# Kernel optimization log

Hardware: AMD Instinct MI355X
Metric: run time of the kernel (lower is better)

## Reference

```python
import jax, jax.numpy as jnp
import numpy as np

B, T, P = 64, 20, 36
V, E, H, D = 32000, 300, 512, 512


def setup_inputs() -> dict:
    key = jax.random.key(0)
    ks = jax.random.split(key, 12)
    s = lambda k, shape, scale=0.05: (jax.random.normal(k, shape, jnp.float32) * scale)
    inp = {
        "h0": jax.random.normal(ks[0], (B, H), jnp.float32),
        "object_proposals": jax.random.normal(ks[1], (B, P, D), jnp.float32),
        "captions": jax.random.randint(ks[2], (B, T), 0, V),
        # lengths in [2, T]; force one row to max so max(decode_lengths) == T-1 (static)
        "caption_lengths": jax.random.randint(ks[3], (B, 1), 2, T + 1).at[0, 0].set(T),
        "emb_W": s(ks[4], (V, E), 0.1),
        "W_ih": s(ks[5], (4 * H, E + D)),
        "W_hh": s(ks[6], (4 * H, H)),
        "b_ih": jnp.zeros((4 * H,), jnp.float32),
        "b_hh": jnp.zeros((4 * H,), jnp.float32),
        "wh_W": s(ks[7], (H, E)), "wh_b": jnp.zeros((H,), jnp.float32),
        "wr_W": s(ks[8], (D, E)), "wr_b": jnp.zeros((D,), jnp.float32),
        "rh_W": s(ks[9], (H, D)), "rh_b": jnp.zeros((H,), jnp.float32),
        "w_W": s(ks[10], (E,)), "w_b": jnp.zeros((), jnp.float32),
        "r_W": s(ks[11], (D,)), "r_b": jnp.zeros((), jnp.float32),
    }
    return inp


def reference(h0, object_proposals, captions, caption_lengths, emb_W,
              W_ih, W_hh, b_ih, b_hh, wh_W, wh_b, wr_W, wr_b,
              rh_W, rh_b, w_W, w_b, r_W, r_b):
    lengths = caption_lengths[:, 0]
    sort_ind = jnp.argsort(-lengths)  # descending, stable
    h0s = h0[sort_ind]
    props = object_proposals[sort_ind]           # [B,P,D]
    caps = captions[sort_ind]                    # [B,T]
    dec = lengths[sort_ind] - 1                  # decode lengths
    Tmax = captions.shape[1] - 1                 # == max(decode_lengths) by construction

    emb = emb_W[caps]                            # [B,T,E]
    # Loop-invariant projections of the full embedding matrix (done once, not per step)
    WH = emb_W @ wh_W.T + wh_b                   # [V,H]
    WRp = emb_W @ wr_W.T + wr_b                  # [V,D]
    w_lin = emb_W @ w_W + w_b                    # [V]
    sum_WH = WH.sum(0)                           # [H]
    sum_WRp = WRp.sum(0)                         # [D]
    sum_wlin = w_lin.sum()                       # scalar
    RH = props @ rh_W.T + rh_b                   # [B,P,H]
    r_lin = props @ r_W + r_b                    # [B,P]
    S = props.sum(1)                             # [B,D]  (sum over proposals)
    wr_sumP = S @ WRp.T                          # [B,V]  = sum_p wr[b,v,p]
    wr_sumV = props @ sum_WRp                    # [B,P]  = sum_v wr[b,v,p]

    xs = (jnp.swapaxes(emb[:, :Tmax], 0, 1), jnp.arange(Tmax))

    def step(carry, x):
        h, c, fb = carry
        e_t, t = x
        mask = (t < dec)[:, None].astype(h.dtype)  # [B,1] active rows
        xin = jnp.concatenate([e_t, fb], axis=1)   # [B,E+D]
        gates = xin @ W_ih.T + b_ih + h @ W_hh.T + b_hh
        i, f, g, o = jnp.split(gates, 4, axis=1)
        c_new = jax.nn.sigmoid(f) * c + jax.nn.sigmoid(i) * jnp.tanh(g)
        h_new = jax.nn.sigmoid(o) * jnp.tanh(c_new)
        w = h_new @ WH.T + w_lin                               # [B,V]
        r = jnp.einsum('bph,bh->bp', RH, h_new) + r_lin        # [B,P]
        preds = w + wr_sumP + r.sum(1, keepdims=True)          # [B,V]
        att_logits = (h_new @ sum_WH + sum_wlin)[:, None] + wr_sumV + r
        att = jax.nn.softmax(att_logits, axis=1)               # [B,P]
        fb_new = jnp.einsum('bp,bpd->bd', att, props)          # [B,D]
        h = mask * h_new + (1.0 - mask) * h
        c = mask * c_new + (1.0 - mask) * c
        fb = mask * fb_new + (1.0 - mask) * fb
        return (h, c, fb), (preds * mask, att * mask)

    init = (h0s, h0s, jnp.zeros((h0.shape[0], props.shape[2]), h0.dtype))
    _, (P_seq, A_seq) = jax.lax.scan(step, init, xs)
    predictions = jnp.swapaxes(P_seq, 0, 1)  # [B,Tmax,V]
    attention = jnp.swapaxes(A_seq, 0, 1)    # [B,Tmax,P]
    return predictions, attention, caps[:, 1:], dec, sort_ind
```

## Files before the change

### kernel.cpp

```cpp
#include <hip/hip_runtime.h>

typedef unsigned short u16;
typedef __bf16 bf16t;
typedef bf16t v8bf __attribute__((ext_vector_type(8)));
typedef float v4f __attribute__((ext_vector_type(4)));

#define Bb 64
#define Tt 20
#define Tm 19
#define Pp 36
#define Vv 32000
#define Ee 300
#define Ep 320
#define Hh 512
#define Dd 512
#define Gg 2048

__device__ __forceinline__ u16 f2b(float f) {
    unsigned u = __builtin_bit_cast(unsigned, f);
    unsigned r = u + 0x7fffu + ((u >> 16) & 1u);
    return (u16)(r >> 16);
}
__device__ __forceinline__ float b2f(u16 x) {
    return __builtin_bit_cast(float, (unsigned)x << 16);
}
__device__ __forceinline__ v8bf ld8(const u16* p) {
    return *reinterpret_cast<const v8bf*>(p);
}

__device__ __forceinline__ float ld_f32_coh(const float* p) {
    return __hip_atomic_load(p, __ATOMIC_RELAXED, __HIP_MEMORY_SCOPE_AGENT);
}
__device__ __forceinline__ void st_f32_coh(float* p, float v) {
    __hip_atomic_store(p, v, __ATOMIC_RELAXED, __HIP_MEMORY_SCOPE_AGENT);
}
__device__ __forceinline__ void st_u32_coh(unsigned* p, unsigned v) {
    __hip_atomic_store(p, v, __ATOMIC_RELAXED, __HIP_MEMORY_SCOPE_AGENT);
}

__global__ void k_sentinel_r4(float* __restrict__ out, float val)
{
    int i = blockIdx.x * 256 + threadIdx.x;
    if (i < 8192) out[i] = val;
}

template<int EPI>
__global__ __launch_bounds__(256) void gemm_bt_r4(
    const u16* __restrict__ A, const u16* __restrict__ B,
    int lda, int ldb, int K,
    float* __restrict__ Cf, u16* __restrict__ Cb, int ldc,
    const float* __restrict__ addN, const float* __restrict__ addM,
    const u16* __restrict__ addMatB,
    const u16* __restrict__ wspB, const int* __restrict__ dec,
    float* __restrict__ outP)
{
    int bn = blockIdx.x, bm = blockIdx.y;
    const int tid = threadIdx.x;
    const int w = tid >> 6, l = tid & 63;
    const int lr = l & 15, lk = (l >> 4) << 3;
    const int m0 = bm * 64;
    const int n0 = bn * 64 + w * 16;
    const u16* Ap = A + (size_t)(m0 + lr) * lda + lk;
    const u16* Bp = B + (size_t)(n0 + lr) * ldb + lk;
    v4f acc0 = {0.f,0.f,0.f,0.f}, acc1 = {0.f,0.f,0.f,0.f},
        acc2 = {0.f,0.f,0.f,0.f}, acc3 = {0.f,0.f,0.f,0.f};
    for (int k = 0; k < K; k += 32) {
        v8bf bf = ld8(Bp + k);
        v8bf a0 = ld8(Ap + k);
        v8bf a1 = ld8(Ap + (size_t)16 * lda + k);
        v8bf a2 = ld8(Ap + (size_t)32 * lda + k);
        v8bf a3 = ld8(Ap + (size_t)48 * lda + k);
        acc0 = __builtin_amdgcn_mfma_f32_16x16x32_bf16(a0, bf, acc0, 0, 0, 0);
        acc1 = __builtin_amdgcn_mfma_f32_16x16x32_bf16(a1, bf, acc1, 0, 0, 0);
        acc2 = __builtin_amdgcn_mfma_f32_16x16x32_bf16(a2, bf, acc2, 0, 0, 0);
        acc3 = __builtin_amdgcn_mfma_f32_16x16x32_bf16(a3, bf, acc3, 0, 0, 0);
    }
    v4f accs[4] = {acc0, acc1, acc2, acc3};
    const int crow0 = (l >> 4) * 4;
    const int n = n0 + lr;
    #pragma unroll
    for (int i = 0; i < 4; ++i) {
        #pragma unroll
        for (int r = 0; r < 4; ++r) {
            int m = m0 + i * 16 + crow0 + r;
            float v = accs[i][r];
            if (EPI == 0) {
                if (addN) v += addN[n];
                Cf[(size_t)m * ldc + n] = v;
            } else if (EPI == 1) {
                Cb[(size_t)m * ldc + n] = f2b(v);
            } else if (EPI == 4) {
                Cb[(size_t)m * ldc + n] = f2b(v + addN[n]);
            } else if (EPI == 5) {
                Cb[(size_t)m * ldc + n] = f2b(v + addM[m]);
            }
        }
    }
}

__global__ __launch_bounds__(256) void k_pred_r10(
    const u16* __restrict__ A,
    const u16* __restrict__ B,
    const float* __restrict__ addN,
    const float* __restrict__ addM,
    const u16* __restrict__ wspB,
    const int* __restrict__ dec,
    float* __restrict__ outP)
{
    const int wg = blockIdx.x;
    const int xcd = wg & 7;
    const int g = wg >> 3;
    const int bn_local = g / 19;
    const int bm = g - bn_local * 19;
    const int nt = (xcd < 5) ? 16 : 15;
    if (bn_local >= nt) return;
    const int bn = ((xcd < 5) ? xcd * 16 : 80 + (xcd - 5) * 15) + bn_local;
    const int t = bm;
    const int n0 = bn * 256;

    __shared__ u16 As[64][72];
    __shared__ u16 Bs[256][72];

    const int tid = threadIdx.x;
    const int w = tid >> 6, l = tid & 63;
    const int lr = l & 15, lk = (l >> 4) << 3;
    const int crow0 = (l >> 4) * 4;

    v4f acc[4][4];
    #pragma unroll
    for (int i = 0; i < 4; ++i)
        #pragma unroll
        for (int j = 0; j < 4; ++j) acc[i][j] = (v4f){0.f,0.f,0.f,0.f};

    for (int kc = 0; kc < 5; ++kc) {
        const int k0 = kc * 64;
        __syncthreads();
        #pragma unroll
        for (int s = 0; s < 2; ++s) {
            int slot = tid + s * 256;
            int row = slot >> 3, c8 = (slot & 7) << 3;
            *reinterpret_cast<v8bf*>(&As[row][c8]) =
                ld8(A + (size_t)(t * 64 + row) * Ep + k0 + c8);
        }
        #pragma unroll
        for (int s = 0; s < 8; ++s) {
            int slot = tid + s * 256;
            int row = slot >> 3, c8 = (slot & 7) << 3;
            *reinterpret_cast<v8bf*>(&Bs[row][c8]) =
                ld8(B + (size_t)(n0 + row) * Ep + k0 + c8);
        }
        __syncthreads();
        #pragma unroll
        for (int ks = 0; ks < 2; ++ks) {
            const int kk = ks * 32 + lk;
            v8bf a0 = *reinterpret_cast<const v8bf*>(&As[lr][kk]);
            v8bf a1 = *reinterpret_cast<const v8bf*>(&As[16 + lr][kk]);
            v8bf a2 = *reinterpret_cast<const v8bf*>(&As[32 + lr][kk]);
            v8bf a3 = *reinterpret_cast<const v8bf*>(&As[48 + lr][kk]);
            #pragma unroll
            for (int j = 0; j < 4; ++j) {
                v8bf bf = *reinterpret_cast<const v8bf*>(&Bs[w * 64 + j * 16 + lr][kk]);
                acc[0][j] = __builtin_amdgcn_mfma_f32_16x16x32_bf16(a0, bf, acc[0][j], 0, 0, 0);
                acc[1][j] = __builtin_amdgcn_mfma_f32_16x16x32_bf16(a1, bf, acc[1][j], 0, 0, 0);
                acc[2][j] = __builtin_amdgcn_mfma_f32_16x16x32_bf16(a2, bf, acc[2][j], 0, 0, 0);
                acc[3][j] = __builtin_amdgcn_mfma_f32_16x16x32_bf16(a3, bf, acc[3][j], 0, 0, 0);
            }
        }
    }

    float aN[4];
    #pragma unroll
    for (int j = 0; j < 4; ++j) aN[j] = addN[n0 + w * 64 + j * 16 + lr];
    #pragma unroll
    for (int i = 0; i < 4; ++i) {
        #pragma unroll
        for (int r = 0; r < 4; ++r) {
            int b = i * 16 + crow0 + r;
            float aM = addM[t * 64 + b];
            bool live = t < dec[b];
            #pragma unroll
            for (int j = 0; j < 4; ++j) {
                int n = n0 + w * 64 + j * 16 + lr;
                float x = aN[j] + aM + b2f(wspB[(size_t)b * Vv + n]);
                float v = acc[i][j][r] + x;
                outP[((size_t)b * Tm + t) * Vv + n] = live ? v : 0.0f;
            }
        }
    }
}

__device__ __forceinline__ void gbar_r7(int* flags, int epoch) {
    __syncthreads();
    if (threadIdx.x == 0)
        __hip_atomic_store(&flags[blockIdx.x * 16], epoch,
                           __ATOMIC_RELAXED, __HIP_MEMORY_SCOPE_AGENT);
    if (threadIdx.x < 64) {
        while (__hip_atomic_load(&flags[threadIdx.x * 16],
                                 __ATOMIC_RELAXED, __HIP_MEMORY_SCOPE_AGENT) < epoch)
            __builtin_amdgcn_s_sleep(1);
    }
    __syncthreads();
}

__global__ __launch_bounds__(256) void k_loop_r12(
    const u16* __restrict__ Wc, const u16* __restrict__ gates_e,
    float* __restrict__ gates,
    const float* __restrict__ sum_WH, const float* __restrict__ sum_wl,
    const float* __restrict__ wr_sumV, const float* __restrict__ r_lin,
    const float* __restrict__ RH, const u16* __restrict__ props_bf,
    const int* __restrict__ dec_i, const float* __restrict__ wh_b,
    const float* __restrict__ h_state, const float* __restrict__ c_state,
    const float* __restrict__ fb_state, u16* __restrict__ xin2s,
    u16* __restrict__ Hseq, float* __restrict__ rsum,
    float* __restrict__ out_att, int* __restrict__ flags)
{
    const int blk = blockIdx.x;
    const int tid = threadIdx.x;
    const int w = tid >> 6, l = tid & 63;
    const int lr = l & 15, lk = (l >> 4) << 3;
    const int m0 = w * 16;
    const int j0 = blk * 32;
    const int crow0 = (l >> 4) * 4;

    __shared__ u16 wldsT[32][2][64][8];
    __shared__ u16 plds[Pp * Dd];
    __shared__ float hbuf[Hh];
    __shared__ float rbuf[Pp];
    __shared__ float attbuf[Pp];
    __shared__ float red1[256], red2[256];
    __shared__ unsigned xbuf32[512];
    u16* xb = (u16*)xbuf32;
    u16* wldsf = (u16*)wldsT;

    #pragma unroll
    for (int s = 0; s < 16; ++s) {
        int slot = tid + s * 256;
        int k = slot >> 7, h = (slot >> 6) & 1, ln = slot & 63;
        *reinterpret_cast<v8bf*>(&wldsf[(size_t)slot * 8]) =
            ld8(Wc + (size_t)(j0 + h * 16 + (ln & 15)) * 1024
                   + k * 32 + ((ln >> 4) << 3));
    }
    for (int idx = tid; idx < (Pp * Dd) / 8; idx += 256) {
        int off = idx << 3;
        *reinterpret_cast<v8bf*>(&plds[off]) =
            ld8(props_bf + (size_t)blk * (Pp * Dd) + off);
    }

    const int b = blk;
    const int dec_b = dec_i[b];
    const float swh0 = sum_WH[tid], swh1 = sum_WH[tid + 256];
    const float wb0 = wh_b[tid], wb1 = wh_b[tid + 256];
    const float sumwl = sum_wl[0];
    const float wrsV = (tid < Pp) ? wr_sumV[b * Pp + tid] : 0.f;
    float rlin[9];
    #pragma unroll
    for (int i = 0; i < 9; ++i) rlin[i] = r_lin[b * Pp + (w + i * 4)];
    float rhv[9][8];
    #pragma unroll
    for (int i = 0; i < 9; ++i) {
        const float* rh = RH + ((size_t)b * Pp + (w + i * 4)) * Dd + l;
        #pragma unroll
        for (int j = 0; j < 8; ++j) rhv[i][j] = rh[j * 64];
    }
    float cr0 = c_state[b * Hh + tid],       cr1 = c_state[b * Hh + tid + 256];
    float hr0 = h_state[b * Hh + tid],       hr1 = h_state[b * Hh + tid + 256];
    float fbr0 = fb_state[b * Hh + tid],     fbr1 = fb_state[b * Hh + tid + 256];
    __syncthreads();

    for (int t = 0; t < Tm; ++t) {
        {
            const u16* Ap = xin2s + (size_t)t * (Bb * 1024)
                                  + (size_t)(m0 + lr) * 1024 + lk;
            v8bf areg[32];
            #pragma unroll
            for (int k = 0; k < 32; ++k) areg[k] = ld8(Ap + k * 32);
            const u16* ge = gates_e + (size_t)t * (Bb * Gg);
            u16 ge0[4], ge1[4];
            size_t obase[4];
            #pragma unroll
            for (int r = 0; r < 4; ++r) {
                int bb = m0 + crow0 + r;
                size_t o0 = (size_t)bb * Gg + j0 + lr;
                obase[r] = o0;
                ge0[r] = ge[o0];
                ge1[r] = ge[o0 + 16];
            }
            v4f acc0 = {0.f,0.f,0.f,0.f}, acc1 = {0.f,0.f,0.f,0.f};
            #pragma unroll
            for (int k = 0; k < 32; ++k) {
                v8bf b0 = *reinterpret_cast<const v8bf*>(&wldsT[k][0][l][0]);
                v8bf b1 = *reinterpret_cast<const v8bf*>(&wldsT[k][1][l][0]);
                acc0 = __builtin_amdgcn_mfma_f32_16x16x32_bf16(areg[k], b0, acc0, 0, 0, 0);
                acc1 = __builtin_amdgcn_mfma_f32_16x16x32_bf16(areg[k], b1, acc1, 0, 0, 0);
            }
            #pragma unroll
            for (int r = 0; r < 4; ++r) {
                st_f32_coh(&gates[obase[r]],      acc0[r] + b2f(ge0[r]));
                st_f32_coh(&gates[obase[r] + 16], acc1[r] + b2f(ge1[r]));
            }
        }
        gbar_r7(flags, 2 * t + 1);
        {
            bool live = t < dec_b;
            float hn_arr[2];
            const float* g = gates + (size_t)b * Gg;
            float gv[8];
            #pragma unroll
            for (int q = 0; q < 2; ++q) {
                int d = tid + q * 256;
                gv[q*4+0] = ld_f32_coh(g + d);
                gv[q*4+1] = ld_f32_coh(g + 512 + d);
                gv[q*4+2] = ld_f32_coh(g + 1024 + d);
                gv[q*4+3] = ld_f32_coh(g + 1536 + d);
            }
            #pragma unroll
            for (int q = 0; q < 2; ++q) {
                int d = tid + q * 256;
                float gi = gv[q*4+0], gf = gv[q*4+1],
                      gg2 = gv[q*4+2], go = gv[q*4+3];
                float c_old = (q == 0) ? cr0 : cr1;
                float si = 1.f / (1.f + expf(-gi));
                float sf = 1.f / (1.f + expf(-gf));
                float so = 1.f / (1.f + expf(-go));
                float cn = sf * c_old + si * tanhf(gg2);
                float hn = so * tanhf(cn);
                hbuf[d] = hn;
                hn_arr[q] = hn;
                Hseq[((size_t)t * Bb + b) * Hh + d] = f2b(hn);
                if (live) {
                    if (q == 0) { cr0 = cn; hr0 = hn; }
                    else        { cr1 = cn; hr1 = hn; }
                }
                xb[Hh + d] = f2b((q == 0) ? hr0 : hr1);
            }
            red1[tid] = hn_arr[0] * swh0 + hn_arr[1] * swh1;
            red2[tid] = hn_arr[0] * wb0 + hn_arr[1] * wb1;
            __syncthreads();
            {
                float hv[8];
                #pragma unroll
                for (int j = 0; j < 8; ++j) hv[j] = hbuf[l + j * 64];
                #pragma unroll
                for (int i = 0; i < 9; ++i) {
                    float a = 0.f;
                    #pragma unroll
                    for (int j = 0; j < 8; ++j) a += rhv[i][j] * hv[j];
                    #pragma unroll
                    for (int off = 32; off > 0; off >>= 1) a += __shfl_down(a, off);
                    if (l == 0) rbuf[w + i * 4] = a + rlin[i];
                }
            }
            __syncthreads();
            for (int s = 128; s > 0; s >>= 1) {
                if (tid < s) { red1[tid] += red1[tid + s]; red2[tid] += red2[tid + s]; }
                __syncthreads();
            }
            if (tid < 64) {
                float hs = red1[0] + sumwl;
                float logit = -3.4e38f;
                if (tid < Pp) logit = hs + wrsV + rbuf[tid];
                float mx = logit;
                for (int off = 32; off > 0; off >>= 1) mx = fmaxf(mx, __shfl_down(mx, off));
                mx = __shfl(mx, 0);
                float ex = (tid < Pp) ? expf(logit - mx) : 0.f;
                float sm = ex;
                for (int off = 32; off > 0; off >>= 1) sm += __shfl_down(sm, off);
                sm = __shfl(sm, 0);
                float att = ex / sm;
                float rs = (tid < Pp) ? rbuf[tid] : 0.f;
                for (int off = 32; off > 0; off >>= 1) rs += __shfl_down(rs, off);
                if (tid == 0) rsum[t * Bb + b] = rs + red2[0];
                if (tid < Pp) {
                    attbuf[tid] = att;
                    out_att[((size_t)b * Tm + t) * Pp + tid] = live ? att : 0.f;
                }
            }
            __syncthreads();
            #pragma unroll
            for (int q = 0; q < 2; ++q) {
                int d = tid + q * 256;
                float fbn = 0.f;
                for (int pp = 0; pp < Pp; ++pp)
                    fbn += attbuf[pp] * b2f(plds[pp * Dd + d]);
                if (live) { if (q == 0) fbr0 = fbn; else fbr1 = fbn; }
                xb[d] = f2b((q == 0) ? fbr0 : fbr1);
            }
            __syncthreads();
            {
                unsigned* xg = (unsigned*)(xin2s + (size_t)(t + 1) * (Bb * 1024)
                                                 + (size_t)b * 1024);
                st_u32_coh(xg + tid, xbuf32[tid]);
                st_u32_coh(xg + tid + 256, xbuf32[tid + 256]);
            }
        }
        gbar_r7(flags, 2 * t + 2);
    }
}

__global__ __launch_bounds__(256) void k_prep1_r12(
    const int* __restrict__ lengths, int* __restrict__ sort_ind,
    int* __restrict__ dec_i, float* __restrict__ out_dec,
    float* __restrict__ out_sort, int* __restrict__ flags,
    const float* __restrict__ b_ih, const float* __restrict__ b_hh,
    float* __restrict__ bias_cat,
    const float* __restrict__ emb_W, const float* __restrict__ w_W,
    const float* __restrict__ w_b, u16* __restrict__ embp,
    float* __restrict__ w_lin,
    const float* __restrict__ W_ih, const float* __restrict__ W_hh,
    u16* __restrict__ Wc, u16* __restrict__ WihE,
    const float* __restrict__ wh_W, const float* __restrict__ wr_W,
    u16* __restrict__ BtWh, u16* __restrict__ BtWr,
    const float* __restrict__ rh_W, u16* __restrict__ rh_bf)
{
    const int blk = blockIdx.x, tid = threadIdx.x;
    if (blk == 0) {
        __shared__ int len[64];
        if (tid < 64) {
            #pragma unroll
            for (int j = 0; j < 16; ++j) flags[tid * 16 + j] = 0;
            len[tid] = lengths[tid];
        }
        __syncthreads();
        if (tid < 64) {
            int li = len[tid];
            int rank = 0;
            for (int j = 0; j < 64; ++j) {
                int lj = len[j];
                rank += (lj > li) || (lj == li && j < tid);
            }
            sort_ind[rank] = tid;
            dec_i[rank] = li - 1;
            out_sort[rank] = (float)tid;
            out_dec[rank] = (float)(li - 1);
        }
    } else if (blk < 9) {
        int j = (blk - 1) * 256 + tid;
        bias_cat[j] = b_ih[j] + b_hh[j];
    } else if (blk < 8009) {
        int v = (blk - 9) * 4 + (tid >> 6);
        int l = tid & 63;
        float acc = 0.f;
        for (int e = l; e < Ep; e += 64) {
            float x = (e < Ee) ? emb_W[(size_t)v * Ee + e] : 0.f;
            embp[(size_t)v * Ep + e] = f2b(x);
            if (e < Ee) acc += x * w_W[e];
        }
        for (int off = 32; off > 0; off >>= 1) acc += __shfl_down(acc, off);
        if (l == 0) w_lin[v] = acc + w_b[0];
    } else if (blk < 8521) {
        int j = (blk - 8009) * 4 + (tid >> 6);
        int l = tid & 63;
        for (int k = l; k < 1024; k += 64) {
            float v = (k < 512) ? W_ih[(size_t)j * 812 + 300 + k]
                                : W_hh[(size_t)j * 512 + (k - 512)];
            Wc[(size_t)j * 1024 + k] = f2b(v);
        }
        for (int e = l; e < Ep; e += 64) {
            float v = (e < Ee) ? W_ih[(size_t)j * 812 + e] : 0.f;
            WihE[(size_t)j * Ep + e] = f2b(v);
        }
    } else if (blk < 9161) {
        int e = blk - 8521;
        const float* W; u16* O;
        if (e < Ep) { W = wh_W; O = BtWh; }
        else { W = wr_W; O = BtWr; e -= Ep; }
        for (int h = tid; h < Hh; h += 256) {
            float v = (e < Ee) ? W[(size_t)h * Ee + e] : 0.f;
            O[(size_t)e * Hh + h] = f2b(v);
        }
    } else {
        int h = (blk - 9161) * 4 + (tid >> 6);
        int l = tid & 63;
        for (int d = l; d < Dd; d += 64)
            rh_bf[(size_t)h * Dd + d] = f2b(rh_W[(size_t)h * Dd + d]);
    }
}


__global__ void k_gather_r4(const float* __restrict__ h0, const int* __restrict__ captions,
                            const int* __restrict__ sort_ind,
                            float* __restrict__ h_state, float* __restrict__ c_state,
                            float* __restrict__ fb_state, u16* __restrict__ xin2,
                            int* __restrict__ caps_s, float* __restrict__ out_caps)
{
    int b = blockIdx.x, tid = threadIdx.x;
    int src = sort_ind[b];
    for (int d = tid; d < Hh; d += 256) {
        float v = h0[(size_t)src * Hh + d];
        h_state[b * Hh + d] = v;
        c_state[b * Hh + d] = v;
        fb_state[b * Hh + d] = 0.f;
        xin2[(size_t)b * 1024 + d] = 0;
        xin2[(size_t)b * 1024 + Hh + d] = f2b(v);
    }
    if (tid < Tt) {
        int cp = captions[src * Tt + tid];
        caps_s[b * Tt + tid] = cp;
        if (tid >= 1) out_caps[b * Tm + (tid - 1)] = (float)cp;
    }
}

__global__ void k_props_r4(const float* __restrict__ props, const int* __restrict__ sort_ind,
                           const float* __restrict__ wr_b,
                           u16* __restrict__ props_bf, u16* __restrict__ S_bf,
                           float* __restrict__ swrb)
{
    int b = blockIdx.x, tid = threadIdx.x;
    int src = sort_ind[b];
    float s0 = 0.f, s1 = 0.f;
    for (int pp = 0; pp < Pp; ++pp) {
        size_t si = ((size_t)src * Pp + pp) * Dd;
        size_t di = ((size_t)b * Pp + pp) * Dd;
        float v0 = props[si + tid];
        float v1 = props[si + tid + 256];
        props_bf[di + tid] = f2b(v0);
        props_bf[di + tid + 256] = f2b(v1);
        s0 += v0; s1 += v1;
    }
    S_bf[b * Dd + tid] = f2b(s0);
    S_bf[b * Dd + tid + 256] = f2b(s1);
    float part = s0 * wr_b[tid] + s1 * wr_b[tid + 256];
    __shared__ float red[256];
    red[tid] = part;
    __syncthreads();
    for (int s = 128; s > 0; s >>= 1) {
        if (tid < s) red[tid] += red[tid + s];
        __syncthreads();
    }
    if (tid == 0) swrb[b] = red[0];
}

__global__ void k_colsumA_r4(const float* __restrict__ emb_W, float* __restrict__ partial)
{
    int blk = blockIdx.x, e = threadIdx.x;
    float s = 0.f;
    int r0 = blk * 100;
    if (e < Ee)
        for (int r = 0; r < 100; ++r) s += emb_W[(size_t)(r0 + r) * Ee + e];
    partial[blk * Ep + e] = (e < Ee) ? s : 0.f;
}

__global__ void k_colsumB_r4(const float* __restrict__ partial, const float* __restrict__ w_W,
                             const float* __restrict__ w_b,
                             float* __restrict__ colsum, float* __restrict__ sum_wl)
{
    int e = threadIdx.x;
    float s = 0.f;
    for (int b = 0; b < 320; ++b) s += partial[b * Ep + e];
    colsum[e] = s;
    __shared__ float red[512];
    red[e] = (e < Ee) ? s * w_W[e] : 0.f;
    if (e < 192) red[320 + e] = 0.f;
    __syncthreads();
    for (int st = 256; st > 0; st >>= 1) {
        if (e < st) red[e] += red[e + st];
        __syncthreads();
    }
    if (e == 0) sum_wl[0] = red[0] + 32000.f * w_b[0];
}

__global__ void k_sums_r4(const float* __restrict__ colsum,
                          const float* __restrict__ wh_W, const float* __restrict__ wh_b,
                          const float* __restrict__ wr_W, const float* __restrict__ wr_b,
                          float* __restrict__ sum_WH, float* __restrict__ sum_WRp)
{
    int g = blockIdx.x * 64 + threadIdx.x;
    const float* W; const float* bias; float* out; int idx;
    if (g < Hh) { W = wh_W; bias = wh_b; out = sum_WH; idx = g; }
    else { W = wr_W; bias = wr_b; out = sum_WRp; idx = g - Hh; }
    float s = 0.f;
    for (int e = 0; e < Ee; ++e) s += colsum[e] * W[(size_t)idx * Ee + e];
    out[idx] = s + 32000.f * bias[idx];
}

__global__ void k_rlin_r4(const u16* __restrict__ props_bf, const float* __restrict__ r_W,
                          const float* __restrict__ r_b, const float* __restrict__ sum_WRp,
                          float* __restrict__ r_lin, float* __restrict__ wr_sumV)
{
    int b = blockIdx.x;
    int w = threadIdx.x >> 6, l = threadIdx.x & 63;
    for (int pp = w; pp < Pp; pp += 4) {
        const u16* row = props_bf + ((size_t)b * Pp + pp) * Dd;
        float a = 0.f, c = 0.f;
        for (int d = l; d < Dd; d += 64) {
            float x = b2f(row[d]);
            a += x * r_W[d];
            c += x * sum_WRp[d];
        }
        for (int off = 32; off > 0; off >>= 1) {
            a += __shfl_down(a, off);
            c += __shfl_down(c, off);
        }
        if (l == 0) {
            r_lin[b * Pp + pp] = a + r_b[0];
            wr_sumV[b * Pp + pp] = c;
        }
    }
}

__global__ void k_embs_r4(const u16* __restrict__ embp, const int* __restrict__ caps_s,
                          u16* __restrict__ emb_s)
{
    int m = blockIdx.x * 4 + (threadIdx.x >> 6);
    int l = threadIdx.x & 63;
    int t = m >> 6, b = m & 63;
    int cap = caps_s[b * Tt + t];
    cap = cap < 0 ? 0 : (cap > Vv - 1 ? Vv - 1 : cap);
    const u16* src = embp + (size_t)cap * Ep;
    u16* dst = emb_s + (size_t)m * Ep;
    for (int e = l; e < Ep; e += 64) dst[e] = src[e];
}

extern "C" void kernel_launch(void* const* d_in, const int* in_sizes, int n_in,
                              void* d_out, int out_size, void* d_ws, size_t ws_size,
                              hipStream_t stream) {
    float* out = (float*)d_out;
    float* out_pred = out;
    float* out_att  = out + (size_t)Bb * Tm * Vv;
    float* out_caps = out_att + (size_t)Bb * Tm * Pp;
    float* out_dec  = out_caps + Bb * Tm;
    float* out_sort = out_dec + Bb;

    if (n_in != 19) {
        k_sentinel_r4<<<32, 256, 0, stream>>>(out_pred, 10240.f);
        return;
    }
    static const int exp_sizes[19] = {
        Bb * Hh, Bb * Pp * Dd, Bb * Tt, Bb, Vv * Ee,
        Gg * (Ee + Dd), Gg * Hh, Gg, Gg,
        Hh * Ee, Hh, Dd * Ee, Dd, Hh * Dd, Hh, Ee, 1, Dd, 1
    };
    for (int i = 0; i < 19; ++i) {
        if (in_sizes[i] != exp_sizes[i]) {
            k_sentinel_r4<<<32, 256, 0, stream>>>(out_pred, 10752.f + 256.f * i);
            return;
        }
    }
    const int exp_out = Bb * Tm * Vv + Bb * Tm * Pp + Bb * Tm + Bb + Bb;
    if (out_size != exp_out) {
        k_sentinel_r4<<<32, 256, 0, stream>>>(out_pred, 11264.f);
        return;
    }

    char* p = (char*)d_ws;
    auto alloc = [&](size_t bytes) -> char* {
        char* r = p;
        p += (bytes + 255) & ~(size_t)255;
        return r;
    };
    int*   i_sort   = (int*)alloc(Bb * 4);
    int*   i_dec    = (int*)alloc(Bb * 4);
    int*   caps_s   = (int*)alloc(Bb * Tt * 4);
    float* h_state  = (float*)alloc(Bb * Hh * 4);
    float* c_state  = (float*)alloc(Bb * Hh * 4);
    float* fb_state = (float*)alloc(Bb * Hh * 4);
    float* swrb     = (float*)alloc(Bb * 4);
    float* gates    = (float*)alloc((size_t)Bb * Gg * 4);
    float* rsum     = (float*)alloc(Tm * Bb * 4);
    float* colsum   = (float*)alloc(Ep * 4);
    float* partialc = (float*)alloc(320 * Ep * 4);
    float* w_lin    = (float*)alloc((size_t)Vv * 4);
    float* sum_WH   = (float*)alloc(Hh * 4);
    float* sum_WRp  = (float*)alloc(Dd * 4);
    float* sum_wl   = (float*)alloc(256);
    float* r_lin    = (float*)alloc(Bb * Pp * 4);
    float* wr_sumV  = (float*)alloc(Bb * Pp * 4);
    float* bias_cat = (float*)alloc(Gg * 4);
    float* RH       = (float*)alloc((size_t)Bb * Pp * Hh * 4);
    int*   flags    = (int*)alloc(Bb * 16 * 4);
    u16*   gates_e  = (u16*)alloc((size_t)Tm * Bb * Gg * 2);
    u16*   wr_sumP  = (u16*)alloc((size_t)Bb * Vv * 2);
    u16*   embp     = (u16*)alloc((size_t)Vv * Ep * 2);
    u16*   emb_s    = (u16*)alloc((size_t)Tm * Bb * Ep * 2);
    u16*   BtWh     = (u16*)alloc((size_t)Ep * Hh * 2);
    u16*   BtWr     = (u16*)alloc((size_t)Ep * Hh * 2);
    u16*   rh_bf    = (u16*)alloc((size_t)Hh * Dd * 2);
    u16*   WihE     = (u16*)alloc((size_t)Gg * Ep * 2);
    u16*   Wc       = (u16*)alloc((size_t)Gg * 1024 * 2);
    u16*   props_bf = (u16*)alloc((size_t)Bb * Pp * Dd * 2);
    u16*   S_bf     = (u16*)alloc(Bb * Dd * 2);
    u16*   Sw       = (u16*)alloc(Bb * Ep * 2);
    u16*   xin2s    = (u16*)alloc((size_t)(Tm + 1) * Bb * 1024 * 2);
    u16*   Hseq     = (u16*)alloc((size_t)Tm * Bb * Hh * 2);
    u16*   Hw       = (u16*)alloc((size_t)Tm * Bb * Ep * 2);
    size_t needed = (size_t)(p - (char*)d_ws);
    if (ws_size < needed) {
        k_sentinel_r4<<<32, 256, 0, stream>>>(out_pred, 10496.f);
        return;
    }

    const float* h0      = (const float*)d_in[0];
    const float* props   = (const float*)d_in[1];
    const int*   captions= (const int*)d_in[2];
    const int*   cap_len = (const int*)d_in[3];
    const float* emb_W   = (const float*)d_in[4];
    const float* W_ih    = (const float*)d_in[5];
    const float* W_hh    = (const float*)d_in[6];
    const float* b_ih    = (const float*)d_in[7];
    const float* b_hh    = (const float*)d_in[8];
    const float* wh_W    = (const float*)d_in[9];
    const float* wh_b    = (const float*)d_in[10];
    const float* wr_W    = (const float*)d_in[11];
    const float* wr_b    = (const float*)d_in[12];
    const float* rh_W    = (const float*)d_in[13];
    const float* rh_b    = (const float*)d_in[14];
    const float* w_W     = (const float*)d_in[15];
    const float* w_b     = (const float*)d_in[16];
    const float* r_W     = (const float*)d_in[17];
    const float* r_b     = (const float*)d_in[18];

    k_prep1_r12<<<9289, 256, 0, stream>>>(
        cap_len, i_sort, i_dec, out_dec, out_sort, flags,
        b_ih, b_hh, bias_cat,
        emb_W, w_W, w_b, embp, w_lin,
        W_ih, W_hh, Wc, WihE,
        wh_W, wr_W, BtWh, BtWr,
        rh_W, rh_bf);
    k_colsumA_r4<<<320, 320, 0, stream>>>(emb_W, partialc);
    k_colsumB_r4<<<1, 320, 0, stream>>>(partialc, w_W, w_b, colsum, sum_wl);
    k_sums_r4<<<16, 64, 0, stream>>>(colsum, wh_W, wh_b, wr_W, wr_b, sum_WH, sum_WRp);
    k_gather_r4<<<Bb, 256, 0, stream>>>(h0, captions, i_sort, h_state, c_state,
                                        fb_state, xin2s, caps_s, out_caps);
    k_props_r4<<<Bb, 256, 0, stream>>>(props, i_sort, wr_b, props_bf, S_bf, swrb);
    k_rlin_r4<<<Bb, 256, 0, stream>>>(props_bf, r_W, r_b, sum_WRp, r_lin, wr_sumV);
    k_embs_r4<<<(Tm * Bb) / 4, 256, 0, stream>>>(embp, caps_s, emb_s);

    gemm_bt_r4<4><<<dim3(Gg / 64, (Tm * Bb) / 64), 256, 0, stream>>>(
        emb_s, WihE, Ep, Ep, Ep, nullptr, gates_e, Gg,
        bias_cat, nullptr, nullptr, nullptr, nullptr, nullptr);
    gemm_bt_r4<0><<<dim3(Hh / 64, (Bb * Pp) / 64), 256, 0, stream>>>(
        props_bf, rh_bf, Dd, Dd, Dd, RH, nullptr, Hh,
        rh_b, nullptr, nullptr, nullptr, nullptr, nullptr);
    gemm_bt_r4<1><<<dim3(Ep / 64, 1), 256, 0, stream>>>(
        S_bf, BtWr, Dd, Hh, Dd, nullptr, Sw, Ep,
        nullptr, nullptr, nullptr, nullptr, nullptr, nullptr);
    gemm_bt_r4<5><<<dim3(Vv / 64, 1), 256, 0, stream>>>(
        Sw, embp, Ep, Ep, Ep, nullptr, wr_sumP, Vv,
        nullptr, swrb, nullptr, nullptr, nullptr, nullptr);

    k_loop_r12<<<Bb, 256, 0, stream>>>(Wc, gates_e, gates, sum_WH, sum_wl, wr_sumV,
                                       r_lin, RH, props_bf, i_dec, wh_b,
                                       h_state, c_state, fb_state, xin2s, Hseq,
                                       rsum, out_att, flags);

    gemm_bt_r4<1><<<dim3(Ep / 64, (Tm * Bb) / 64), 256, 0, stream>>>(
        Hseq, BtWh, Hh, Hh, Hh, nullptr, Hw, Ep,
        nullptr, nullptr, nullptr, nullptr, nullptr, nullptr);
    k_pred_r10<<<dim3(8 * 304), 256, 0, stream>>>(
        Hw, embp, w_lin, rsum, wr_sumP, i_dec, out_pred);
}
```

Before: 641.4 us.

## Merge prep kernels into four fused launches and fold Hseq GEMM into loop

Roughly twelve small preprocessing launches (colsum, gather, props, sums, rlin, embedding gather and four GEMMs) are packed into four multi-role kernels that dispatch on block index, grouped by dependency level. The Hseq×BtWh projection GEMM now runs at the tail of the persistent recurrent loop kernel over its 64 blocks, with Hseq written through coherent packed stores so the data is visible after the final grid barrier. This removes launch gaps and serialization between many tiny kernels. In exchange, the tail GEMM runs on only 64 blocks instead of a full grid.

```diff
diff --git a/kernel.cpp b/kernel.cpp
--- a/kernel.cpp
+++ b/kernel.cpp
@@ -45,16 +45,13 @@
 }
 
 template<int EPI>
-__global__ __launch_bounds__(256) void gemm_bt_r4(
+__device__ __forceinline__ void gemm_body(
+    int bn, int bm,
     const u16* __restrict__ A, const u16* __restrict__ B,
     int lda, int ldb, int K,
     float* __restrict__ Cf, u16* __restrict__ Cb, int ldc,
-    const float* __restrict__ addN, const float* __restrict__ addM,
-    const u16* __restrict__ addMatB,
-    const u16* __restrict__ wspB, const int* __restrict__ dec,
-    float* __restrict__ outP)
+    const float* __restrict__ addN, const float* __restrict__ addM)
 {
-    int bn = blockIdx.x, bm = blockIdx.y;
     const int tid = threadIdx.x;
     const int w = tid >> 6, l = tid & 63;
     const int lr = l & 15, lk = (l >> 4) << 3;
@@ -85,7 +82,7 @@
             int m = m0 + i * 16 + crow0 + r;
             float v = accs[i][r];
             if (EPI == 0) {
-                if (addN) v += addN[n];
+                v += addN[n];
                 Cf[(size_t)m * ldc + n] = v;
             } else if (EPI == 1) {
                 Cb[(size_t)m * ldc + n] = f2b(v);
@@ -202,7 +199,7 @@
     __syncthreads();
 }
 
-__global__ __launch_bounds__(256) void k_loop_r12(
+__global__ __launch_bounds__(256) void k_loop_r13(
     const u16* __restrict__ Wc, const u16* __restrict__ gates_e,
     float* __restrict__ gates,
     const float* __restrict__ sum_WH, const float* __restrict__ sum_wl,
@@ -212,7 +209,8 @@
     const float* __restrict__ h_state, const float* __restrict__ c_state,
     const float* __restrict__ fb_state, u16* __restrict__ xin2s,
     u16* __restrict__ Hseq, float* __restrict__ rsum,
-    float* __restrict__ out_att, int* __restrict__ flags)
+    float* __restrict__ out_att, int* __restrict__ flags,
+    const u16* __restrict__ BtWh, u16* __restrict__ Hw)
 {
     const int blk = blockIdx.x;
     const int tid = threadIdx.x;
@@ -326,7 +324,6 @@
                 float hn = so * tanhf(cn);
                 hbuf[d] = hn;
                 hn_arr[q] = hn;
-                Hseq[((size_t)t * Bb + b) * Hh + d] = f2b(hn);
                 if (live) {
                     if (q == 0) { cr0 = cn; hr0 = hn; }
                     else        { cr1 = cn; hr1 = hn; }
@@ -336,6 +333,12 @@
             red1[tid] = hn_arr[0] * swh0 + hn_arr[1] * swh1;
             red2[tid] = hn_arr[0] * wb0 + hn_arr[1] * wb1;
             __syncthreads();
+            {
+                unsigned* hrow = (unsigned*)(Hseq + ((size_t)t * Bb + b) * Hh);
+                unsigned lo = f2b(hbuf[2 * tid]);
+                unsigned hi = f2b(hbuf[2 * tid + 1]);
+                st_u32_coh(hrow + tid, lo | (hi << 16));
+            }
             {
                 float hv[8];
                 #pragma unroll
@@ -395,9 +398,15 @@
         }
         gbar_r7(flags, 2 * t + 2);
     }
-}
-
-__global__ __launch_bounds__(256) void k_prep1_r12(
+
+    for (int tau = blk; tau < 5 * Tm; tau += Bb) {
+        int bm = tau / 5, bn = tau - bm * 5;
+        gemm_body<1>(bn, bm, Hseq, BtWh, Hh, Hh, Hh,
+                     nullptr, Hw, Ep, nullptr, nullptr);
+    }
+}
+
+__global__ __launch_bounds__(256) void k_prepA_r13(
     const int* __restrict__ lengths, int* __restrict__ sort_ind,
     int* __restrict__ dec_i, float* __restrict__ out_dec,
     float* __restrict__ out_sort, int* __restrict__ flags,
@@ -410,22 +419,23 @@
     u16* __restrict__ Wc, u16* __restrict__ WihE,
     const float* __restrict__ wh_W, const float* __restrict__ wr_W,
     u16* __restrict__ BtWh, u16* __restrict__ BtWr,
-    const float* __restrict__ rh_W, u16* __restrict__ rh_bf)
+    const float* __restrict__ rh_W, u16* __restrict__ rh_bf,
+    float* __restrict__ partialc)
 {
     const int blk = blockIdx.x, tid = threadIdx.x;
+    __shared__ int ilen[64];
     if (blk == 0) {
-        __shared__ int len[64];
         if (tid < 64) {
             #pragma unroll
             for (int j = 0; j < 16; ++j) flags[tid * 16 + j] = 0;
-            len[tid] = lengths[tid];
+            ilen[tid] = lengths[tid];
         }
         __syncthreads();
         if (tid < 64) {
-            int li = len[tid];
+            int li = ilen[tid];
             int rank = 0;
             for (int j = 0; j < 64; ++j) {
-                int lj = len[j];
+                int lj = ilen[j];
                 rank += (lj > li) || (lj == li && j < tid);
             }
             sort_ind[rank] = tid;
@@ -468,147 +478,179 @@
             float v = (e < Ee) ? W[(size_t)h * Ee + e] : 0.f;
             O[(size_t)e * Hh + h] = f2b(v);
         }
-    } else {
+    } else if (blk < 9289) {
         int h = (blk - 9161) * 4 + (tid >> 6);
         int l = tid & 63;
         for (int d = l; d < Dd; d += 64)
             rh_bf[(size_t)h * Dd + d] = f2b(rh_W[(size_t)h * Dd + d]);
-    }
-}
-
-
-__global__ void k_gather_r4(const float* __restrict__ h0, const int* __restrict__ captions,
-                            const int* __restrict__ sort_ind,
-                            float* __restrict__ h_state, float* __restrict__ c_state,
-                            float* __restrict__ fb_state, u16* __restrict__ xin2,
-                            int* __restrict__ caps_s, float* __restrict__ out_caps)
+    } else {
+        int cb = blk - 9289;
+        int r0 = cb * 100;
+        for (int e = tid; e < Ep; e += 256) {
+            float s = 0.f;
+            if (e < Ee)
+                for (int r = 0; r < 100; ++r) s += emb_W[(size_t)(r0 + r) * Ee + e];
+            partialc[cb * Ep + e] = (e < Ee) ? s : 0.f;
+        }
+    }
+}
+
+__global__ __launch_bounds__(256) void k_prepB_r13(
+    const float* __restrict__ partialc, const float* __restrict__ w_W,
+    const float* __restrict__ w_b, float* __restrict__ colsum,
+    float* __restrict__ sum_wl,
+    const float* __restrict__ h0, const int* __restrict__ captions,
+    const int* __restrict__ sort_ind,
+    float* __restrict__ h_state, float* __restrict__ c_state,
+    float* __restrict__ fb_state, u16* __restrict__ xin2,
+    int* __restrict__ caps_s, float* __restrict__ out_caps,
+    const float* __restrict__ props, const float* __restrict__ wr_b,
+    u16* __restrict__ props_bf, u16* __restrict__ S_bf,
+    float* __restrict__ swrb)
 {
-    int b = blockIdx.x, tid = threadIdx.x;
-    int src = sort_ind[b];
-    for (int d = tid; d < Hh; d += 256) {
-        float v = h0[(size_t)src * Hh + d];
-        h_state[b * Hh + d] = v;
-        c_state[b * Hh + d] = v;
-        fb_state[b * Hh + d] = 0.f;
-        xin2[(size_t)b * 1024 + d] = 0;
-        xin2[(size_t)b * 1024 + Hh + d] = f2b(v);
-    }
-    if (tid < Tt) {
-        int cp = captions[src * Tt + tid];
-        caps_s[b * Tt + tid] = cp;
-        if (tid >= 1) out_caps[b * Tm + (tid - 1)] = (float)cp;
-    }
-}
-
-__global__ void k_props_r4(const float* __restrict__ props, const int* __restrict__ sort_ind,
-                           const float* __restrict__ wr_b,
-                           u16* __restrict__ props_bf, u16* __restrict__ S_bf,
-                           float* __restrict__ swrb)
+    const int blk = blockIdx.x, tid = threadIdx.x;
+    __shared__ float sred[512];
+    if (blk == 0) {
+        int e2 = tid + 256;
+        float s1 = 0.f, s2 = 0.f;
+        for (int cb = 0; cb < 320; ++cb) {
+            s1 += partialc[cb * Ep + tid];
+            if (e2 < Ep) s2 += partialc[cb * Ep + e2];
+        }
+        colsum[tid] = s1;
+        if (e2 < Ep) colsum[e2] = s2;
+        sred[tid] = s1 * w_W[tid];
+        sred[e2] = (e2 < Ee) ? s2 * w_W[e2] : 0.f;
+        __syncthreads();
+        for (int st = 256; st > 0; st >>= 1) {
+            if (tid < st) sred[tid] += sred[tid + st];
+            __syncthreads();
+        }
+        if (tid == 0) sum_wl[0] = sred[0] + 32000.f * w_b[0];
+    } else if (blk < 65) {
+        int b = blk - 1;
+        int src = sort_ind[b];
+        for (int d = tid; d < Hh; d += 256) {
+            float v = h0[(size_t)src * Hh + d];
+            h_state[b * Hh + d] = v;
+            c_state[b * Hh + d] = v;
+            fb_state[b * Hh + d] = 0.f;
+            xin2[(size_t)b * 1024 + d] = 0;
+            xin2[(size_t)b * 1024 + Hh + d] = f2b(v);
+        }
+        if (tid < Tt) {
+            int cp = captions[src * Tt + tid];
+            caps_s[b * Tt + tid] = cp;
+            if (tid >= 1) out_caps[b * Tm + (tid - 1)] = (float)cp;
+        }
+    } else {
+        int b = blk - 65;
+        int src = sort_ind[b];
+        float s0 = 0.f, s1 = 0.f;
+        for (int pp = 0; pp < Pp; ++pp) {
+            size_t si = ((size_t)src * Pp + pp) * Dd;
+            size_t di = ((size_t)b * Pp + pp) * Dd;
+            float v0 = props[si + tid];
+            float v1 = props[si + tid + 256];
+            props_bf[di + tid] = f2b(v0);
+            props_bf[di + tid + 256] = f2b(v1);
+            s0 += v0; s1 += v1;
+        }
+        S_bf[b * Dd + tid] = f2b(s0);
+        S_bf[b * Dd + tid + 256] = f2b(s1);
+        float part = s0 * wr_b[tid] + s1 * wr_b[tid + 256];
+        sred[tid] = part;
+        __syncthreads();
+        for (int s = 128; s > 0; s >>= 1) {
+            if (tid < s) sred[tid] += sred[tid + s];
+            __syncthreads();
+        }
+        if (tid == 0) swrb[b] = sred[0];
+    }
+}
+
+__global__ __launch_bounds__(256) void k_prepC_r13(
+    const float* __restrict__ colsum,
+    const float* __restrict__ wh_W, const float* __restrict__ wh_b,
+    const float* __restrict__ wr_W, const float* __restrict__ wr_b,
+    float* __restrict__ sum_WH, float* __restrict__ sum_WRp,
+    const u16* __restrict__ embp, const int* __restrict__ caps_s,
+    u16* __restrict__ emb_s,
+    const u16* __restrict__ props_bf, const u16* __restrict__ rh_bf,
+    const float* __restrict__ rh_b, float* __restrict__ RH,
+    const u16* __restrict__ S_bf, const u16* __restrict__ BtWr,
+    u16* __restrict__ Sw)
 {
-    int b = blockIdx.x, tid = threadIdx.x;
-    int src = sort_ind[b];
-    float s0 = 0.f, s1 = 0.f;
-    for (int pp = 0; pp < Pp; ++pp) {
-        size_t si = ((size_t)src * Pp + pp) * Dd;
-        size_t di = ((size_t)b * Pp + pp) * Dd;
-        float v0 = props[si + tid];
-        float v1 = props[si + tid + 256];
-        props_bf[di + tid] = f2b(v0);
-        props_bf[di + tid + 256] = f2b(v1);
-        s0 += v0; s1 += v1;
-    }
-    S_bf[b * Dd + tid] = f2b(s0);
-    S_bf[b * Dd + tid + 256] = f2b(s1);
-    float part = s0 * wr_b[tid] + s1 * wr_b[tid + 256];
-    __shared__ float red[256];
-    red[tid] = part;
-    __syncthreads();
-    for (int s = 128; s > 0; s >>= 1) {
-        if (tid < s) red[tid] += red[tid + s];
-        __syncthreads();
-    }
-    if (tid == 0) swrb[b] = red[0];
-}
-
-__global__ void k_colsumA_r4(const float* __restrict__ emb_W, float* __restrict__ partial)
+    const int blk = blockIdx.x, tid = threadIdx.x;
+    if (blk < 4) {
+        int g = blk * 256 + tid;
+        const float* W; const float* bias; float* out; int idx;
+        if (g < Hh) { W = wh_W; bias = wh_b; out = sum_WH; idx = g; }
+        else { W = wr_W; bias = wr_b; out = sum_WRp; idx = g - Hh; }
+        float s = 0.f;
+        for (int e = 0; e < Ee; ++e) s += colsum[e] * W[(size_t)idx * Ee + e];
+        out[idx] = s + 32000.f * bias[idx];
+    } else if (blk < 308) {
+        int m = (blk - 4) * 4 + (tid >> 6);
+        int l = tid & 63;
+        int t = m >> 6, b = m & 63;
+        int cap = caps_s[b * Tt + t];
+        cap = cap < 0 ? 0 : (cap > Vv - 1 ? Vv - 1 : cap);
+        const u16* src = embp + (size_t)cap * Ep;
+        u16* dst = emb_s + (size_t)m * Ep;
+        for (int e = l; e < Ep; e += 64) dst[e] = src[e];
+    } else if (blk < 596) {
+        int tau = blk - 308;
+        int bn = tau & 7, bm = tau >> 3;
+        gemm_body<0>(bn, bm, props_bf, rh_bf, Dd, Dd, Dd,
+                     RH, nullptr, Hh, rh_b, nullptr);
+    } else {
+        int bn = blk - 596;
+        gemm_body<1>(bn, 0, S_bf, BtWr, Dd, Hh, Dd,
+                     nullptr, Sw, Ep, nullptr, nullptr);
+    }
+}
+
+__global__ __launch_bounds__(256) void k_prepD_r13(
+    const u16* __restrict__ props_bf, const float* __restrict__ r_W,
+    const float* __restrict__ r_b, const float* __restrict__ sum_WRp,
+    float* __restrict__ r_lin, float* __restrict__ wr_sumV,
+    const u16* __restrict__ emb_s, const u16* __restrict__ WihE,
+    const float* __restrict__ bias_cat, u16* __restrict__ gates_e,
+    const u16* __restrict__ Sw, const u16* __restrict__ embp,
+    const float* __restrict__ swrb, u16* __restrict__ wr_sumP)
 {
-    int blk = blockIdx.x, e = threadIdx.x;
-    float s = 0.f;
-    int r0 = blk * 100;
-    if (e < Ee)
-        for (int r = 0; r < 100; ++r) s += emb_W[(size_t)(r0 + r) * Ee + e];
-    partial[blk * Ep + e] = (e < Ee) ? s : 0.f;
-}
-
-__global__ void k_colsumB_r4(const float* __restrict__ partial, const float* __restrict__ w_W,
-                             const float* __restrict__ w_b,
-                             float* __restrict__ colsum, float* __restrict__ sum_wl)
-{
-    int e = threadIdx.x;
-    float s = 0.f;
-    for (int b = 0; b < 320; ++b) s += partial[b * Ep + e];
-    colsum[e] = s;
-    __shared__ float red[512];
-    red[e] = (e < Ee) ? s * w_W[e] : 0.f;
-    if (e < 192) red[320 + e] = 0.f;
-    __syncthreads();
-    for (int st = 256; st > 0; st >>= 1) {
-        if (e < st) red[e] += red[e + st];
-        __syncthreads();
-    }
-    if (e == 0) sum_wl[0] = red[0] + 32000.f * w_b[0];
-}
-
-__global__ void k_sums_r4(const float* __restrict__ colsum,
-                          const float* __restrict__ wh_W, const float* __restrict__ wh_b,
-                          const float* __restrict__ wr_W, const float* __restrict__ wr_b,
-                          float* __restrict__ sum_WH, float* __restrict__ sum_WRp)
-{
-    int g = blockIdx.x * 64 + threadIdx.x;
-    const float* W; const float* bias; float* out; int idx;
-    if (g < Hh) { W = wh_W; bias = wh_b; out = sum_WH; idx = g; }
-    else { W = wr_W; bias = wr_b; out = sum_WRp; idx = g - Hh; }
-    float s = 0.f;
-    for (int e = 0; e < Ee; ++e) s += colsum[e] * W[(size_t)idx * Ee + e];
-    out[idx] = s + 32000.f * bias[idx];
-}
-
-__global__ void k_rlin_r4(const u16* __restrict__ props_bf, const float* __restrict__ r_W,
-                          const float* __restrict__ r_b, const float* __restrict__ sum_WRp,
-                          float* __restrict__ r_lin, float* __restrict__ wr_sumV)
-{
-    int b = blockIdx.x;
-    int w = threadIdx.x >> 6, l = threadIdx.x & 63;
-    for (int pp = w; pp < Pp; pp += 4) {
-        const u16* row = props_bf + ((size_t)b * Pp + pp) * Dd;
-        float a = 0.f, c = 0.f;
-        for (int d = l; d < Dd; d += 64) {
-            float x = b2f(row[d]);
-            a += x * r_W[d];
-            c += x * sum_WRp[d];
-        }
-        for (int off = 32; off > 0; off >>= 1) {
-            a += __shfl_down(a, off);
-            c += __shfl_down(c, off);
-        }
-        if (l == 0) {
-            r_lin[b * Pp + pp] = a + r_b[0];
-            wr_sumV[b * Pp + pp] = c;
-        }
-    }
-}
-
-__global__ void k_embs_r4(const u16* __restrict__ embp, const int* __restrict__ caps_s,
-                          u16* __restrict__ emb_s)
-{
-    int m = blockIdx.x * 4 + (threadIdx.x >> 6);
-    int l = threadIdx.x & 63;
-    int t = m >> 6, b = m & 63;
-    int cap = caps_s[b * Tt + t];
-    cap = cap < 0 ? 0 : (cap > Vv - 1 ? Vv - 1 : cap);
-    const u16* src = embp + (size_t)cap * Ep;
-    u16* dst = emb_s + (size_t)m * Ep;
-    for (int e = l; e < Ep; e += 64) dst[e] = src[e];
+    const int blk = blockIdx.x, tid = threadIdx.x;
+    if (blk < 64) {
+        int b = blk;
+        int w = tid >> 6, l = tid & 63;
+        for (int pp = w; pp < Pp; pp += 4) {
+            const u16* row = props_bf + ((size_t)b * Pp + pp) * Dd;
+            float a = 0.f, c = 0.f;
+            for (int d = l; d < Dd; d += 64) {
+                float x = b2f(row[d]);
+                a += x * r_W[d];
+                c += x * sum_WRp[d];
+            }
+            for (int off = 32; off > 0; off >>= 1) {
+                a += __shfl_down(a, off);
+                c += __shfl_down(c, off);
+            }
+            if (l == 0) {
+                r_lin[b * Pp + pp] = a + r_b[0];
+                wr_sumV[b * Pp + pp] = c;
+            }
+        }
+    } else if (blk < 672) {
+        int tau = blk - 64;
+        int bn = tau & 31, bm = tau >> 5;
+        gemm_body<4>(bn, bm, emb_s, WihE, Ep, Ep, Ep,
+                     nullptr, gates_e, Gg, bias_cat, nullptr);
+    } else {
+        int bn = blk - 672;
+        gemm_body<5>(bn, 0, Sw, embp, Ep, Ep, Ep,
+                     nullptr, wr_sumP, Vv, nullptr, swrb);
+    }
 }
 
 extern "C" void kernel_launch(void* const* d_in, const int* in_sizes, int n_in,
@@ -709,43 +751,33 @@
     const float* r_W     = (const float*)d_in[17];
     const float* r_b     = (const float*)d_in[18];
 
-    k_prep1_r12<<<9289, 256, 0, stream>>>(
+    k_prepA_r13<<<9609, 256, 0, stream>>>(
         cap_len, i_sort, i_dec, out_dec, out_sort, flags,
         b_ih, b_hh, bias_cat,
         emb_W, w_W, w_b, embp, w_lin,
         W_ih, W_hh, Wc, WihE,
         wh_W, wr_W, BtWh, BtWr,
-        rh_W, rh_bf);
-    k_colsumA_r4<<<320, 320, 0, stream>>>(emb_W, partialc);
-    k_colsumB_r4<<<1, 320, 0, stream>>>(partialc, w_W, w_b, colsum, sum_wl);
-    k_sums_r4<<<16, 64, 0, stream>>>(colsum, wh_W, wh_b, wr_W, wr_b, sum_WH, sum_WRp);
-    k_gather_r4<<<Bb, 256, 0, stream>>>(h0, captions, i_sort, h_state, c_state,
-                                        fb_state, xin2s, caps_s, out_caps);
-    k_props_r4<<<Bb, 256, 0, stream>>>(props, i_sort, wr_b, props_bf, S_bf, swrb);
-    k_rlin_r4<<<Bb, 256, 0, stream>>>(props_bf, r_W, r_b, sum_WRp, r_lin, wr_sumV);
-    k_embs_r4<<<(Tm * Bb) / 4, 256, 0, stream>>>(embp, caps_s, emb_s);
-
-    gemm_bt_r4<4><<<dim3(Gg / 64, (Tm * Bb) / 64), 256, 0, stream>>>(
-        emb_s, WihE, Ep, Ep, Ep, nullptr, gates_e, Gg,
-        bias_cat, nullptr, nullptr, nullptr, nullptr, nullptr);
-    gemm_bt_r4<0><<<dim3(Hh / 64, (Bb * Pp) / 64), 256, 0, stream>>>(
-        props_bf, rh_bf, Dd, Dd, Dd, RH, nullptr, Hh,
-        rh_b, nullptr, nullptr, nullptr, nullptr, nullptr);
-    gemm_bt_r4<1><<<dim3(Ep / 64, 1), 256, 0, stream>>>(
-        S_bf, BtWr, Dd, Hh, Dd, nullptr, Sw, Ep,
-        nullptr, nullptr, nullptr, nullptr, nullptr, nullptr);
-    gemm_bt_r4<5><<<dim3(Vv / 64, 1), 256, 0, stream>>>(
-        Sw, embp, Ep, Ep, Ep, nullptr, wr_sumP, Vv,
-        nullptr, swrb, nullptr, nullptr, nullptr, nullptr);
-
-    k_loop_r12<<<Bb, 256, 0, stream>>>(Wc, gates_e, gates, sum_WH, sum_wl, wr_sumV,
+        rh_W, rh_bf, partialc);
+    k_prepB_r13<<<129, 256, 0, stream>>>(
+        partialc, w_W, w_b, colsum, sum_wl,
+        h0, captions, i_sort, h_state, c_state, fb_state, xin2s,
+        caps_s, out_caps,
+        props, wr_b, props_bf, S_bf, swrb);
+    k_prepC_r13<<<601, 256, 0, stream>>>(
+        colsum, wh_W, wh_b, wr_W, wr_b, sum_WH, sum_WRp,
+        embp, caps_s, emb_s,
+        props_bf, rh_bf, rh_b, RH,
+        S_bf, BtWr, Sw);
+    k_prepD_r13<<<1172, 256, 0, stream>>>(
+        props_bf, r_W, r_b, sum_WRp, r_lin, wr_sumV,
+        emb_s, WihE, bias_cat, gates_e,
+        Sw, embp, swrb, wr_sumP);
+
+    k_loop_r13<<<Bb, 256, 0, stream>>>(Wc, gates_e, gates, sum_WH, sum_wl, wr_sumV,
                                        r_lin, RH, props_bf, i_dec, wh_b,
                                        h_state, c_state, fb_state, xin2s, Hseq,
-                                       rsum, out_att, flags);
-
-    gemm_bt_r4<1><<<dim3(Ep / 64, (Tm * Bb) / 64), 256, 0, stream>>>(
-        Hseq, BtWh, Hh, Hh, Hh, nullptr, Hw, Ep,
-        nullptr, nullptr, nullptr, nullptr, nullptr, nullptr);
+                                       rsum, out_att, flags, BtWh, Hw);
+
     k_pred_r10<<<dim3(8 * 304), 256, 0, stream>>>(
         Hw, embp, w_lin, rsum, wr_sumP, i_dec, out_pred);
 }
```

Result: slower. 665.5 us (+3.8%).
